# Kernel tuning notes

Hardware: AMD Instinct MI355X
Metric: run time of the kernel (lower is better)

## Reference

```python
import jax, jax.numpy as jnp
import numpy as np

EPS = 1e-5
LOGIT_DIM = 16   # 2**arity, arity=4
HID = 128        # circuit_hidden_dim == pe_dim
MSG = LOGIT_DIM + HID  # 144


def layer_norm(x, scale, bias):
    mu = jnp.mean(x, axis=-1, keepdims=True)
    var = jnp.mean(jnp.square(x - mu), axis=-1, keepdims=True)
    return (x - mu) * jax.lax.rsqrt(var + EPS) * scale + bias


def setup_inputs() -> dict:
    key = jax.random.key(0)
    N = 200000
    ks = jax.random.split(key, 16)
    inp = {
        'logits': jax.random.normal(ks[0], (N, LOGIT_DIM), jnp.float32),
        'hidden': jax.random.normal(ks[1], (N, HID), jnp.float32),
        'layer_pe': jax.random.normal(ks[2], (N, HID), jnp.float32),
        'intra_layer_pe': jax.random.normal(ks[3], (N, HID), jnp.float32),
        'loss': jax.random.normal(ks[4], (N,), jnp.float32),
        'layer': jax.random.randint(ks[5], (N,), 0, 8, jnp.int32),
        'sent_attributes': jax.random.normal(ks[6], (N, MSG), jnp.float32),
    }
    # LayerNorm params (scale=1, bias=0 as flax default init)
    for name, d in [('logits', LOGIT_DIM), ('hidden', HID), ('layer_pe', HID),
                    ('intra_pe', HID), ('loss', 1), ('msg', MSG)]:
        inp[f'ln_{name}_s'] = jnp.ones((d,), jnp.float32)
        inp[f'ln_{name}_b'] = jnp.zeros((d,), jnp.float32)
    # MLP: 545 -> 256 (LN, relu) -> 256 (LN, relu) -> 144
    D_IN = LOGIT_DIM + HID + HID + HID + 1 + MSG  # 545
    inp['W0'] = jax.random.normal(ks[7], (D_IN, 256), jnp.float32) * 0.02
    inp['b0'] = jnp.zeros((256,), jnp.float32)
    inp['mlp_ln0_s'] = jnp.ones((256,), jnp.float32)
    inp['mlp_ln0_b'] = jnp.zeros((256,), jnp.float32)
    inp['W1'] = jax.random.normal(ks[8], (256, 256), jnp.float32) * 0.02
    inp['b1'] = jnp.zeros((256,), jnp.float32)
    inp['mlp_ln1_s'] = jnp.ones((256,), jnp.float32)
    inp['mlp_ln1_b'] = jnp.zeros((256,), jnp.float32)
    inp['W2'] = jax.random.normal(ks[9], (256, MSG), jnp.float32) * 0.02
    inp['b2'] = jnp.zeros((MSG,), jnp.float32)
    return inp


def reference(logits, hidden, layer_pe, intra_layer_pe, loss, layer, sent_attributes,
              ln_logits_s, ln_logits_b, ln_hidden_s, ln_hidden_b,
              ln_layer_pe_s, ln_layer_pe_b, ln_intra_pe_s, ln_intra_pe_b,
              ln_loss_s, ln_loss_b, ln_msg_s, ln_msg_b,
              W0, b0, mlp_ln0_s, mlp_ln0_b, W1, b1, mlp_ln1_s, mlp_ln1_b, W2, b2):
    # Five field-wise LayerNorms + message LayerNorm, then concat
    x = jnp.concatenate([
        layer_norm(logits, ln_logits_s, ln_logits_b),
        layer_norm(hidden, ln_hidden_s, ln_hidden_b),
        layer_norm(layer_pe, ln_layer_pe_s, ln_layer_pe_b),
        layer_norm(intra_layer_pe, ln_intra_pe_s, ln_intra_pe_b),
        layer_norm(loss[:, None], ln_loss_s, ln_loss_b),
        layer_norm(sent_attributes, ln_msg_s, ln_msg_b),
    ], axis=-1)  # [N, 545]
    # MLP: Linear + LN + relu (x2), final Linear
    h = jax.nn.relu(layer_norm(x @ W0 + b0, mlp_ln0_s, mlp_ln0_b))
    h = jax.nn.relu(layer_norm(h @ W1 + b1, mlp_ln1_s, mlp_ln1_b))
    delta = h @ W2 + b2  # [N, 144]
    delta_logits = delta[..., :LOGIT_DIM]
    delta_hidden = delta[..., LOGIT_DIM:]
    # Masked residual: only gate nodes (layer > 0) are updated; scales are 1.0
    mask = (layer > 0)[:, None]
    updated_logits = jnp.where(mask, logits + delta_logits, logits)
    updated_hidden = jnp.where(mask, hidden + delta_hidden, hidden)
    return jnp.concatenate([updated_logits, updated_hidden], axis=-1)  # [N, 144]
```

## Files before the change

kernel.cpp:

```cpp
#include <hip/hip_runtime.h>
#include <hip/hip_bf16.h>

#define EPSV 1e-5f
#define BM   32
#define XSTR 552
#define DSTR 276

using bf16x8 = __attribute__((ext_vector_type(8))) short;
using f32x4  = __attribute__((ext_vector_type(4))) float;
using us4    = __attribute__((ext_vector_type(4))) unsigned short;
using us8    = __attribute__((ext_vector_type(8))) unsigned short;

__device__ __forceinline__ unsigned short f2bf(float f) {
    unsigned int u = __float_as_uint(f);
    u += 0x7fffu + ((u >> 16) & 1u);
    return (unsigned short)(u >> 16);
}

__device__ __forceinline__ int orig_row(int k) {
    return (k < 144) ? k : ((k < 288) ? (k + 257) : (k - 144));
}
__device__ __forceinline__ float seg_pick(int k,
    const float* a, const float* b, const float* c, const float* d, const float* e) {
    if (k < 16)  return a[k];
    if (k < 144) return b[k - 16];
    if (k < 288) return c[k - 144];
    if (k < 416) return d[k - 288];
    return e[k - 416];
}

__global__ void prep_kernel(const float* __restrict__ W0, const float* __restrict__ b0,
                            const float* __restrict__ ln_loss_b,
                            const float* __restrict__ W1, const float* __restrict__ W2,
                            const float* __restrict__ ls_s, const float* __restrict__ hs_s,
                            const float* __restrict__ ms_s, const float* __restrict__ pe_s,
                            const float* __restrict__ in_s,
                            const float* __restrict__ ls_b, const float* __restrict__ hs_b,
                            const float* __restrict__ ms_b, const float* __restrict__ pe_b,
                            const float* __restrict__ in_b,
                            unsigned short* __restrict__ W0p, unsigned short* __restrict__ W1p,
                            unsigned short* __restrict__ W2p, float* __restrict__ b0e)
{
    int gtid = blockIdx.x * blockDim.x + threadIdx.x;
    if (gtid < 17408) {
        int lane = gtid & 63, fid = gtid >> 6;
        int s = fid >> 4, t = fid & 15;
        int n  = (t << 4) + (lane & 15);
        int kb = (s << 5) + ((lane >> 4) << 3);
        us8 v;
        #pragma unroll
        for (int i = 0; i < 8; ++i) {
            int k = kb + i;
            float sc = seg_pick(k, ls_s, hs_s, ms_s, pe_s, in_s);
            v[i] = f2bf(sc * W0[orig_row(k) * 256 + n]);
        }
        *reinterpret_cast<us8*>(W0p + gtid * 8) = v;
    } else if (gtid < 17408 + 8192) {
        int g = gtid - 17408;
        int lane = g & 63, fid = g >> 6;
        int s = fid >> 4, t = fid & 15;
        int n  = (t << 4) + (lane & 15);
        int kb = (s << 5) + ((lane >> 4) << 3);
        us8 v;
        #pragma unroll
        for (int i = 0; i < 8; ++i) v[i] = f2bf(W1[(kb + i) * 256 + n]);
        *reinterpret_cast<us8*>(W1p + g * 8) = v;
    } else if (gtid < 17408 + 8192 + 4608) {
        int g = gtid - 17408 - 8192;
        int lane = g & 63, fid = g >> 6;
        int s = fid / 9, t = fid % 9;
        int n  = (t << 4) + (lane & 15);
        int kb = (s << 5) + ((lane >> 4) << 3);
        us8 v;
        #pragma unroll
        for (int i = 0; i < 8; ++i) v[i] = f2bf(W2[(kb + i) * 144 + n]);
        *reinterpret_cast<us8*>(W2p + g * 8) = v;
    } else if (gtid < 17408 + 8192 + 4608 + 8192) {
        int idx = gtid - (17408 + 8192 + 4608);
        int n   = idx >> 5;
        int sub = idx & 31;
        float acc = 0.f;
        #pragma unroll
        for (int j = 0; j < 17; ++j) {
            int k = sub + 32 * j;
            float bb = seg_pick(k, ls_b, hs_b, ms_b, pe_b, in_b);
            acc += bb * W0[orig_row(k) * 256 + n];
        }
        acc += __shfl_xor(acc, 1);  acc += __shfl_xor(acc, 2);
        acc += __shfl_xor(acc, 4);  acc += __shfl_xor(acc, 8);
        acc += __shfl_xor(acc, 16);
        if (sub == 0)
            b0e[n] = acc + b0[n] + ln_loss_b[0] * W0[400 * 256 + n];
    }
}

template<int L>
__device__ __forceinline__ void stage8(
    const float* __restrict__ src,
    unsigned short* xb, int dstcol, int tid, int row0)
{
    constexpr int SPAN = L / 8;
    const int sub = tid & 7;
    const int r   = tid >> 3;
    const float* p = src + (size_t)(row0 + r) * L + sub * SPAN;
    float ps = 0.f, pq = 0.f;
    if constexpr (SPAN % 4 == 0) {
        constexpr int NV = SPAN / 4;
        float4 v[NV];
        #pragma unroll
        for (int j = 0; j < NV; ++j) {
            v[j] = *reinterpret_cast<const float4*>(p + 4 * j);
            ps += v[j].x + v[j].y + v[j].z + v[j].w;
            pq += v[j].x * v[j].x + v[j].y * v[j].y + v[j].z * v[j].z + v[j].w * v[j].w;
        }
        ps += __shfl_xor(ps, 1); ps += __shfl_xor(ps, 2); ps += __shfl_xor(ps, 4);
        pq += __shfl_xor(pq, 1); pq += __shfl_xor(pq, 2); pq += __shfl_xor(pq, 4);
        const float mu   = ps * (1.f / L);
        const float rstd = rsqrtf(pq * (1.f / L) - mu * mu + EPSV);
        unsigned short* dst = xb + r * XSTR + dstcol + sub * SPAN;
        #pragma unroll
        for (int j = 0; j < NV; ++j) {
            us4 o;
            o[0] = f2bf((v[j].x - mu) * rstd);
            o[1] = f2bf((v[j].y - mu) * rstd);
            o[2] = f2bf((v[j].z - mu) * rstd);
            o[3] = f2bf((v[j].w - mu) * rstd);
            *reinterpret_cast<us4*>(dst + 4 * j) = o;
        }
    } else {
        constexpr int NV = SPAN / 2;
        float2 v[NV];
        #pragma unroll
        for (int j = 0; j < NV; ++j) {
            v[j] = *reinterpret_cast<const float2*>(p + 2 * j);
            ps += v[j].x + v[j].y;
            pq += v[j].x * v[j].x + v[j].y * v[j].y;
        }
        ps += __shfl_xor(ps, 1); ps += __shfl_xor(ps, 2); ps += __shfl_xor(ps, 4);
        pq += __shfl_xor(pq, 1); pq += __shfl_xor(pq, 2); pq += __shfl_xor(pq, 4);
        const float mu   = ps * (1.f / L);
        const float rstd = rsqrtf(pq * (1.f / L) - mu * mu + EPSV);
        unsigned short* dst = xb + r * XSTR + dstcol + sub * SPAN;
        #pragma unroll
        for (int j = 0; j < NV; ++j) {
            unsigned int pk = (unsigned int)f2bf((v[j].x - mu) * rstd)
                            | ((unsigned int)f2bf((v[j].y - mu) * rstd) << 16);
            *reinterpret_cast<unsigned int*>(dst + 2 * j) = pk;
        }
    }
}

__global__ __launch_bounds__(256, 4) void node_update_kernel(
    const float* __restrict__ logits, const float* __restrict__ hidden,
    const float* __restrict__ layer_pe, const float* __restrict__ intra,
    const int* __restrict__ layer, const float* __restrict__ msg,
    const unsigned short* __restrict__ W0p, const float* __restrict__ b0e,
    const float* __restrict__ mlp_ln0_s, const float* __restrict__ mlp_ln0_b,
    const unsigned short* __restrict__ W1p, const float* __restrict__ b1,
    const float* __restrict__ mlp_ln1_s, const float* __restrict__ mlp_ln1_b,
    const unsigned short* __restrict__ W2p, const float* __restrict__ b2,
    float* __restrict__ out)
{
    __shared__ __align__(16) unsigned short sbuf[BM * XSTR];
    __shared__ __align__(16) float redf[BM * 4 * 2];
    __shared__ int lyr[BM];

    float2* redp = reinterpret_cast<float2*>(redf);
    const float4* redq = reinterpret_cast<const float4*>(redf);
    const int tid  = threadIdx.x;
    const int lane = tid & 63;
    const int w    = tid >> 6;
    const int l15  = lane & 15;
    const int lg   = lane >> 4;
    const int row0 = blockIdx.x * BM;

    stage8<16 >(logits,   sbuf,   0, tid, row0);
    stage8<128>(hidden,   sbuf,  16, tid, row0);
    stage8<144>(msg,      sbuf, 144, tid, row0);
    stage8<128>(layer_pe, sbuf, 288, tid, row0);
    stage8<128>(intra,    sbuf, 416, tid, row0);
    if (tid < BM) lyr[tid] = layer[row0 + tid];
    __syncthreads();

    f32x4 acc[2][4];
    #pragma unroll
    for (int m = 0; m < 2; ++m)
        #pragma unroll
        for (int t = 0; t < 4; ++t)
            acc[m][t] = (f32x4){0.f, 0.f, 0.f, 0.f};

    for (int s = 0; s < 17; ++s) {
        bf16x8 a[2];
        #pragma unroll
        for (int m = 0; m < 2; ++m)
            a[m] = *reinterpret_cast<const bf16x8*>(&sbuf[(16 * m + l15) * XSTR + 32 * s + 8 * lg]);
        #pragma unroll
        for (int t = 0; t < 4; ++t) {
            bf16x8 b = *reinterpret_cast<const bf16x8*>(W0p + (((s * 16 + w * 4 + t) * 64 + lane) << 3));
            #pragma unroll
            for (int m = 0; m < 2; ++m)
                acc[m][t] = __builtin_amdgcn_mfma_f32_16x16x32_bf16(a[m], b, acc[m][t], 0, 0, 0);
        }
    }

    {
        float bv[4], sv[4], bb[4];
        #pragma unroll
        for (int t = 0; t < 4; ++t) {
            int n = w * 64 + t * 16 + l15;
            bv[t] = b0e[n]; sv[t] = mlp_ln0_s[n]; bb[t] = mlp_ln0_b[n];
        }
        #pragma unroll
        for (int m = 0; m < 2; ++m)
            #pragma unroll
            for (int t = 0; t < 4; ++t)
                #pragma unroll
                for (int i = 0; i < 4; ++i)
                    acc[m][t][i] += bv[t];
        #pragma unroll
        for (int m = 0; m < 2; ++m) {
            #pragma unroll
            for (int i = 0; i < 4; ++i) {
                float ps = acc[m][0][i] + acc[m][1][i] + acc[m][2][i] + acc[m][3][i];
                float pq = acc[m][0][i] * acc[m][0][i] + acc[m][1][i] * acc[m][1][i]
                         + acc[m][2][i] * acc[m][2][i] + acc[m][3][i] * acc[m][3][i];
                ps += __shfl_xor(ps, 1); ps += __shfl_xor(ps, 2); ps += __shfl_xor(ps, 4); ps += __shfl_xor(ps, 8);
                pq += __shfl_xor(pq, 1); pq += __shfl_xor(pq, 2); pq += __shfl_xor(pq, 4); pq += __shfl_xor(pq, 8);
                if (l15 == 0) redp[(16 * m + 4 * lg + i) * 4 + w] = make_float2(ps, pq);
            }
        }
        __syncthreads();
        #pragma unroll
        for (int m = 0; m < 2; ++m)
            #pragma unroll
            for (int i = 0; i < 4; ++i) {
                int r = 16 * m + 4 * lg + i;
                float4 q0 = redq[r * 2 + 0], q1 = redq[r * 2 + 1];
                float s  = q0.x + q0.z + q1.x + q1.z;
                float q  = q0.y + q0.w + q1.y + q1.w;
                float mu = s * (1.f / 256.f);
                float rstd = rsqrtf(q * (1.f / 256.f) - mu * mu + EPSV);
                #pragma unroll
                for (int t = 0; t < 4; ++t) {
                    float y = (acc[m][t][i] - mu) * rstd * sv[t] + bb[t];
                    sbuf[r * XSTR + w * 64 + t * 16 + l15] = f2bf(fmaxf(y, 0.f));
                }
            }
    }
    __syncthreads();

    #pragma unroll
    for (int m = 0; m < 2; ++m)
        #pragma unroll
        for (int t = 0; t < 4; ++t)
            acc[m][t] = (f32x4){0.f, 0.f, 0.f, 0.f};
    for (int s = 0; s < 8; ++s) {
        bf16x8 a[2];
        #pragma unroll
        for (int m = 0; m < 2; ++m)
            a[m] = *reinterpret_cast<const bf16x8*>(&sbuf[(16 * m + l15) * XSTR + 32 * s + 8 * lg]);
        #pragma unroll
        for (int t = 0; t < 4; ++t) {
            bf16x8 b = *reinterpret_cast<const bf16x8*>(W1p + (((s * 16 + w * 4 + t) * 64 + lane) << 3));
            #pragma unroll
            for (int m = 0; m < 2; ++m)
                acc[m][t] = __builtin_amdgcn_mfma_f32_16x16x32_bf16(a[m], b, acc[m][t], 0, 0, 0);
        }
    }

    {
        float bv[4], sv[4], bb[4];
        #pragma unroll
        for (int t = 0; t < 4; ++t) {
            int n = w * 64 + t * 16 + l15;
            bv[t] = b1[n]; sv[t] = mlp_ln1_s[n]; bb[t] = mlp_ln1_b[n];
        }
        #pragma unroll
        for (int m = 0; m < 2; ++m)
            #pragma unroll
            for (int t = 0; t < 4; ++t)
                #pragma unroll
                for (int i = 0; i < 4; ++i)
                    acc[m][t][i] += bv[t];
        #pragma unroll
        for (int m = 0; m < 2; ++m) {
            #pragma unroll
            for (int i = 0; i < 4; ++i) {
                float ps = acc[m][0][i] + acc[m][1][i] + acc[m][2][i] + acc[m][3][i];
                float pq = acc[m][0][i] * acc[m][0][i] + acc[m][1][i] * acc[m][1][i]
                         + acc[m][2][i] * acc[m][2][i] + acc[m][3][i] * acc[m][3][i];
                ps += __shfl_xor(ps, 1); ps += __shfl_xor(ps, 2); ps += __shfl_xor(ps, 4); ps += __shfl_xor(ps, 8);
                pq += __shfl_xor(pq, 1); pq += __shfl_xor(pq, 2); pq += __shfl_xor(pq, 4); pq += __shfl_xor(pq, 8);
                if (l15 == 0) redp[(16 * m + 4 * lg + i) * 4 + w] = make_float2(ps, pq);
            }
        }
        __syncthreads();
        #pragma unroll
        for (int m = 0; m < 2; ++m)
            #pragma unroll
            for (int i = 0; i < 4; ++i) {
                int r = 16 * m + 4 * lg + i;
                float4 q0 = redq[r * 2 + 0], q1 = redq[r * 2 + 1];
                float s  = q0.x + q0.z + q1.x + q1.z;
                float q  = q0.y + q0.w + q1.y + q1.w;
                float mu = s * (1.f / 256.f);
                float rstd = rsqrtf(q * (1.f / 256.f) - mu * mu + EPSV);
                #pragma unroll
                for (int t = 0; t < 4; ++t) {
                    float y = (acc[m][t][i] - mu) * rstd * sv[t] + bb[t];
                    sbuf[r * XSTR + w * 64 + t * 16 + l15] = f2bf(fmaxf(y, 0.f));
                }
            }
    }
    __syncthreads();

    {
        const int rg = w & 1;
        const int ch = w >> 1;
        const unsigned short* arow = sbuf + (16 * rg + l15) * XSTR;
        float* delta = reinterpret_cast<float*>(sbuf);
        if (ch == 0) {
            f32x4 acc3[5];
            #pragma unroll
            for (int t = 0; t < 5; ++t) acc3[t] = (f32x4){0.f, 0.f, 0.f, 0.f};
            for (int s = 0; s < 8; ++s) {
                bf16x8 a = *reinterpret_cast<const bf16x8*>(arow + 32 * s + 8 * lg);
                #pragma unroll
                for (int t = 0; t < 5; ++t) {
                    bf16x8 b = *reinterpret_cast<const bf16x8*>(W2p + (((s * 9 + t) * 64 + lane) << 3));
                    acc3[t] = __builtin_amdgcn_mfma_f32_16x16x32_bf16(a, b, acc3[t], 0, 0, 0);
                }
            }
            __syncthreads();
            #pragma unroll
            for (int t = 0; t < 5; ++t)
                #pragma unroll
                for (int i = 0; i < 4; ++i)
                    delta[(16 * rg + 4 * lg + i) * DSTR + 16 * t + l15] = acc3[t][i];
        } else {
            f32x4 acc3[4];
            #pragma unroll
            for (int t = 0; t < 4; ++t) acc3[t] = (f32x4){0.f, 0.f, 0.f, 0.f};
            for (int s = 0; s < 8; ++s) {
                bf16x8 a = *reinterpret_cast<const bf16x8*>(arow + 32 * s + 8 * lg);
                #pragma unroll
                for (int t = 0; t < 4; ++t) {
                    bf16x8 b = *reinterpret_cast<const bf16x8*>(W2p + (((s * 9 + t + 5) * 64 + lane) << 3));
                    acc3[t] = __builtin_amdgcn_mfma_f32_16x16x32_bf16(a, b, acc3[t], 0, 0, 0);
                }
            }
            __syncthreads();
            #pragma unroll
            for (int t = 0; t < 4; ++t)
                #pragma unroll
                for (int i = 0; i < 4; ++i)
                    delta[(16 * rg + 4 * lg + i) * DSTR + 16 * (t + 5) + l15] = acc3[t][i];
        }
    }
    __syncthreads();

    const float* delta = reinterpret_cast<const float*>(sbuf);
    #pragma unroll
    for (int j = 0; j < 5; ++j) {
        int idx = tid + j * 256;
        if (idx < BM * 36) {
            int r = idx / 36, c4 = idx % 36;
            int grow = row0 + r;
            float4 d  = *reinterpret_cast<const float4*>(delta + r * DSTR + 4 * c4);
            float4 bb = *reinterpret_cast<const float4*>(b2 + 4 * c4);
            float4 base;
            if (c4 < 4) base = *reinterpret_cast<const float4*>(logits + (size_t)grow * 16 + 4 * c4);
            else        base = *reinterpret_cast<const float4*>(hidden + (size_t)grow * 128 + 4 * c4 - 16);
            const bool mk = lyr[r] > 0;
            f32x4 o;
            o[0] = mk ? base.x + d.x + bb.x : base.x;
            o[1] = mk ? base.y + d.y + bb.y : base.y;
            o[2] = mk ? base.z + d.z + bb.z : base.z;
            o[3] = mk ? base.w + d.w + bb.w : base.w;
            __builtin_nontemporal_store(o, reinterpret_cast<f32x4*>(out + (size_t)grow * 144 + 4 * c4));
        }
    }
}

extern "C" void kernel_launch(void* const* d_in, const int* in_sizes, int n_in,
                              void* d_out, int out_size, void* d_ws, size_t ws_size,
                              hipStream_t stream)
{
    const float* logits        = (const float*)d_in[0];
    const float* hidden        = (const float*)d_in[1];
    const float* layer_pe      = (const float*)d_in[2];
    const float* intra         = (const float*)d_in[3];
    const int*   layer         = (const int*)  d_in[5];
    const float* msg           = (const float*)d_in[6];
    const float* ln_logits_s   = (const float*)d_in[7];
    const float* ln_logits_b   = (const float*)d_in[8];
    const float* ln_hidden_s   = (const float*)d_in[9];
    const float* ln_hidden_b   = (const float*)d_in[10];
    const float* ln_layer_pe_s = (const float*)d_in[11];
    const float* ln_layer_pe_b = (const float*)d_in[12];
    const float* ln_intra_pe_s = (const float*)d_in[13];
    const float* ln_intra_pe_b = (const float*)d_in[14];
    const float* ln_loss_b     = (const float*)d_in[16];
    const float* ln_msg_s      = (const float*)d_in[17];
    const float* ln_msg_b      = (const float*)d_in[18];
    const float* W0            = (const float*)d_in[19];
    const float* b0            = (const float*)d_in[20];
    const float* mlp_ln0_s     = (const float*)d_in[21];
    const float* mlp_ln0_b     = (const float*)d_in[22];
    const float* W1            = (const float*)d_in[23];
    const float* b1            = (const float*)d_in[24];
    const float* mlp_ln1_s     = (const float*)d_in[25];
    const float* mlp_ln1_b     = (const float*)d_in[26];
    const float* W2            = (const float*)d_in[27];
    const float* b2            = (const float*)d_in[28];
    float* out = (float*)d_out;

    unsigned short* W0p = (unsigned short*)d_ws;
    unsigned short* W1p = (unsigned short*)((char*)d_ws + 278528);
    unsigned short* W2p = (unsigned short*)((char*)d_ws + 409600);
    float*          b0e = (float*)((char*)d_ws + 483328);

    prep_kernel<<<150, 256, 0, stream>>>(W0, b0, ln_loss_b, W1, W2,
        ln_logits_s, ln_hidden_s, ln_msg_s, ln_layer_pe_s, ln_intra_pe_s,
        ln_logits_b, ln_hidden_b, ln_msg_b, ln_layer_pe_b, ln_intra_pe_b,
        W0p, W1p, W2p, b0e);

    const int N = in_sizes[5];
    node_update_kernel<<<N / BM, 256, 0, stream>>>(
        logits, hidden, layer_pe, intra, layer, msg,
        W0p, b0e, mlp_ln0_s, mlp_ln0_b,
        W1p, b1, mlp_ln1_s, mlp_ln1_b,
        W2p, b2, out);
}
```

Before: 280.0 us.

## Double block to 512 threads, split N columns across eight waves

The block grows from 4 to 8 waves for the same 32-row tile. Each wave now owns 32 output columns instead of 64 in the first two GEMMs, and the final 144-column GEMM is split 3/2/2/2 tiles across column groups. Staging now uses 16 threads per row with coalesced float4 strides, and the LayerNorm reduction buffer widens to 8 partials per row. The aim is more waves in flight to hide global-load and MFMA latency, at the cost of more barrier participants and reduction overhead.

Measured after the change: 293.5 us. 4.8% more time.

```diff
diff --git a/kernel.cpp b/kernel.cpp
--- a/kernel.cpp
+++ b/kernel.cpp
@@ -95,62 +95,47 @@
 }
 
 template<int L>
-__device__ __forceinline__ void stage8(
+__device__ __forceinline__ void stage16(
     const float* __restrict__ src,
     unsigned short* xb, int dstcol, int tid, int row0)
 {
-    constexpr int SPAN = L / 8;
-    const int sub = tid & 7;
-    const int r   = tid >> 3;
-    const float* p = src + (size_t)(row0 + r) * L + sub * SPAN;
+    constexpr int NJ  = L / 64;
+    constexpr int REM = L - NJ * 64;
+    const int sub = tid & 15;
+    const int r   = tid >> 4;
+    const float* rowp = src + (size_t)(row0 + r) * L;
+    float4 v[NJ > 0 ? NJ : 1];
+    float  vr = 0.f;
     float ps = 0.f, pq = 0.f;
-    if constexpr (SPAN % 4 == 0) {
-        constexpr int NV = SPAN / 4;
-        float4 v[NV];
-        #pragma unroll
-        for (int j = 0; j < NV; ++j) {
-            v[j] = *reinterpret_cast<const float4*>(p + 4 * j);
-            ps += v[j].x + v[j].y + v[j].z + v[j].w;
-            pq += v[j].x * v[j].x + v[j].y * v[j].y + v[j].z * v[j].z + v[j].w * v[j].w;
-        }
-        ps += __shfl_xor(ps, 1); ps += __shfl_xor(ps, 2); ps += __shfl_xor(ps, 4);
-        pq += __shfl_xor(pq, 1); pq += __shfl_xor(pq, 2); pq += __shfl_xor(pq, 4);
-        const float mu   = ps * (1.f / L);
-        const float rstd = rsqrtf(pq * (1.f / L) - mu * mu + EPSV);
-        unsigned short* dst = xb + r * XSTR + dstcol + sub * SPAN;
-        #pragma unroll
-        for (int j = 0; j < NV; ++j) {
-            us4 o;
-            o[0] = f2bf((v[j].x - mu) * rstd);
-            o[1] = f2bf((v[j].y - mu) * rstd);
-            o[2] = f2bf((v[j].z - mu) * rstd);
-            o[3] = f2bf((v[j].w - mu) * rstd);
-            *reinterpret_cast<us4*>(dst + 4 * j) = o;
-        }
-    } else {
-        constexpr int NV = SPAN / 2;
-        float2 v[NV];
-        #pragma unroll
-        for (int j = 0; j < NV; ++j) {
-            v[j] = *reinterpret_cast<const float2*>(p + 2 * j);
-            ps += v[j].x + v[j].y;
-            pq += v[j].x * v[j].x + v[j].y * v[j].y;
-        }
-        ps += __shfl_xor(ps, 1); ps += __shfl_xor(ps, 2); ps += __shfl_xor(ps, 4);
-        pq += __shfl_xor(pq, 1); pq += __shfl_xor(pq, 2); pq += __shfl_xor(pq, 4);
-        const float mu   = ps * (1.f / L);
-        const float rstd = rsqrtf(pq * (1.f / L) - mu * mu + EPSV);
-        unsigned short* dst = xb + r * XSTR + dstcol + sub * SPAN;
-        #pragma unroll
-        for (int j = 0; j < NV; ++j) {
-            unsigned int pk = (unsigned int)f2bf((v[j].x - mu) * rstd)
-                            | ((unsigned int)f2bf((v[j].y - mu) * rstd) << 16);
-            *reinterpret_cast<unsigned int*>(dst + 2 * j) = pk;
-        }
-    }
-}
-
-__global__ __launch_bounds__(256, 4) void node_update_kernel(
+    #pragma unroll
+    for (int j = 0; j < NJ; ++j) {
+        v[j] = *reinterpret_cast<const float4*>(rowp + 4 * sub + 64 * j);
+        ps += v[j].x + v[j].y + v[j].z + v[j].w;
+        pq += v[j].x * v[j].x + v[j].y * v[j].y + v[j].z * v[j].z + v[j].w * v[j].w;
+    }
+    if constexpr (REM) {
+        vr = rowp[64 * NJ + sub];
+        ps += vr; pq += vr * vr;
+    }
+    ps += __shfl_xor(ps, 1); ps += __shfl_xor(ps, 2); ps += __shfl_xor(ps, 4); ps += __shfl_xor(ps, 8);
+    pq += __shfl_xor(pq, 1); pq += __shfl_xor(pq, 2); pq += __shfl_xor(pq, 4); pq += __shfl_xor(pq, 8);
+    const float mu   = ps * (1.f / L);
+    const float rstd = rsqrtf(pq * (1.f / L) - mu * mu + EPSV);
+    unsigned short* dstrow = xb + r * XSTR + dstcol;
+    #pragma unroll
+    for (int j = 0; j < NJ; ++j) {
+        us4 o;
+        o[0] = f2bf((v[j].x - mu) * rstd);
+        o[1] = f2bf((v[j].y - mu) * rstd);
+        o[2] = f2bf((v[j].z - mu) * rstd);
+        o[3] = f2bf((v[j].w - mu) * rstd);
+        *reinterpret_cast<us4*>(dstrow + 4 * sub + 64 * j) = o;
+    }
+    if constexpr (REM)
+        dstrow[64 * NJ + sub] = f2bf((vr - mu) * rstd);
+}
+
+__global__ __launch_bounds__(512, 6) void node_update_kernel(
     const float* __restrict__ logits, const float* __restrict__ hidden,
     const float* __restrict__ layer_pe, const float* __restrict__ intra,
     const int* __restrict__ layer, const float* __restrict__ msg,
@@ -162,7 +147,7 @@
     float* __restrict__ out)
 {
     __shared__ __align__(16) unsigned short sbuf[BM * XSTR];
-    __shared__ __align__(16) float redf[BM * 4 * 2];
+    __shared__ __align__(16) float redf[BM * 8 * 2];
     __shared__ int lyr[BM];
 
     float2* redp = reinterpret_cast<float2*>(redf);
@@ -174,19 +159,19 @@
     const int lg   = lane >> 4;
     const int row0 = blockIdx.x * BM;
 
-    stage8<16 >(logits,   sbuf,   0, tid, row0);
-    stage8<128>(hidden,   sbuf,  16, tid, row0);
-    stage8<144>(msg,      sbuf, 144, tid, row0);
-    stage8<128>(layer_pe, sbuf, 288, tid, row0);
-    stage8<128>(intra,    sbuf, 416, tid, row0);
+    stage16<16 >(logits,   sbuf,   0, tid, row0);
+    stage16<128>(hidden,   sbuf,  16, tid, row0);
+    stage16<144>(msg,      sbuf, 144, tid, row0);
+    stage16<128>(layer_pe, sbuf, 288, tid, row0);
+    stage16<128>(intra,    sbuf, 416, tid, row0);
     if (tid < BM) lyr[tid] = layer[row0 + tid];
     __syncthreads();
 
-    f32x4 acc[2][4];
+    f32x4 acc[2][2];
     #pragma unroll
     for (int m = 0; m < 2; ++m)
         #pragma unroll
-        for (int t = 0; t < 4; ++t)
+        for (int t = 0; t < 2; ++t)
             acc[m][t] = (f32x4){0.f, 0.f, 0.f, 0.f};
 
     for (int s = 0; s < 17; ++s) {
@@ -195,8 +180,8 @@
         for (int m = 0; m < 2; ++m)
             a[m] = *reinterpret_cast<const bf16x8*>(&sbuf[(16 * m + l15) * XSTR + 32 * s + 8 * lg]);
         #pragma unroll
-        for (int t = 0; t < 4; ++t) {
-            bf16x8 b = *reinterpret_cast<const bf16x8*>(W0p + (((s * 16 + w * 4 + t) * 64 + lane) << 3));
+        for (int t = 0; t < 2; ++t) {
+            bf16x8 b = *reinterpret_cast<const bf16x8*>(W0p + (((s * 16 + w * 2 + t) * 64 + lane) << 3));
             #pragma unroll
             for (int m = 0; m < 2; ++m)
                 acc[m][t] = __builtin_amdgcn_mfma_f32_16x16x32_bf16(a[m], b, acc[m][t], 0, 0, 0);
@@ -204,16 +189,16 @@
     }
 
     {
-        float bv[4], sv[4], bb[4];
-        #pragma unroll
-        for (int t = 0; t < 4; ++t) {
-            int n = w * 64 + t * 16 + l15;
+        float bv[2], sv[2], bb[2];
+        #pragma unroll
+        for (int t = 0; t < 2; ++t) {
+            int n = w * 32 + t * 16 + l15;
             bv[t] = b0e[n]; sv[t] = mlp_ln0_s[n]; bb[t] = mlp_ln0_b[n];
         }
         #pragma unroll
         for (int m = 0; m < 2; ++m)
             #pragma unroll
-            for (int t = 0; t < 4; ++t)
+            for (int t = 0; t < 2; ++t)
                 #pragma unroll
                 for (int i = 0; i < 4; ++i)
                     acc[m][t][i] += bv[t];
@@ -221,12 +206,11 @@
         for (int m = 0; m < 2; ++m) {
             #pragma unroll
             for (int i = 0; i < 4; ++i) {
-                float ps = acc[m][0][i] + acc[m][1][i] + acc[m][2][i] + acc[m][3][i];
-                float pq = acc[m][0][i] * acc[m][0][i] + acc[m][1][i] * acc[m][1][i]
-                         + acc[m][2][i] * acc[m][2][i] + acc[m][3][i] * acc[m][3][i];
+                float ps = acc[m][0][i] + acc[m][1][i];
+                float pq = acc[m][0][i] * acc[m][0][i] + acc[m][1][i] * acc[m][1][i];
                 ps += __shfl_xor(ps, 1); ps += __shfl_xor(ps, 2); ps += __shfl_xor(ps, 4); ps += __shfl_xor(ps, 8);
                 pq += __shfl_xor(pq, 1); pq += __shfl_xor(pq, 2); pq += __shfl_xor(pq, 4); pq += __shfl_xor(pq, 8);
-                if (l15 == 0) redp[(16 * m + 4 * lg + i) * 4 + w] = make_float2(ps, pq);
+                if (l15 == 0) redp[(16 * m + 4 * lg + i) * 8 + w] = make_float2(ps, pq);
             }
         }
         __syncthreads();
@@ -235,15 +219,16 @@
             #pragma unroll
             for (int i = 0; i < 4; ++i) {
                 int r = 16 * m + 4 * lg + i;
-                float4 q0 = redq[r * 2 + 0], q1 = redq[r * 2 + 1];
-                float s  = q0.x + q0.z + q1.x + q1.z;
-                float q  = q0.y + q0.w + q1.y + q1.w;
+                float4 q0 = redq[r * 4 + 0], q1 = redq[r * 4 + 1];
+                float4 q2 = redq[r * 4 + 2], q3 = redq[r * 4 + 3];
+                float s  = q0.x + q0.z + q1.x + q1.z + q2.x + q2.z + q3.x + q3.z;
+                float q  = q0.y + q0.w + q1.y + q1.w + q2.y + q2.w + q3.y + q3.w;
                 float mu = s * (1.f / 256.f);
                 float rstd = rsqrtf(q * (1.f / 256.f) - mu * mu + EPSV);
                 #pragma unroll
-                for (int t = 0; t < 4; ++t) {
+                for (int t = 0; t < 2; ++t) {
                     float y = (acc[m][t][i] - mu) * rstd * sv[t] + bb[t];
-                    sbuf[r * XSTR + w * 64 + t * 16 + l15] = f2bf(fmaxf(y, 0.f));
+                    sbuf[r * XSTR + w * 32 + t * 16 + l15] = f2bf(fmaxf(y, 0.f));
                 }
             }
     }
@@ -252,7 +237,7 @@
     #pragma unroll
     for (int m = 0; m < 2; ++m)
         #pragma unroll
-        for (int t = 0; t < 4; ++t)
+        for (int t = 0; t < 2; ++t)
             acc[m][t] = (f32x4){0.f, 0.f, 0.f, 0.f};
     for (int s = 0; s < 8; ++s) {
         bf16x8 a[2];
@@ -260,8 +245,8 @@
         for (int m = 0; m < 2; ++m)
             a[m] = *reinterpret_cast<const bf16x8*>(&sbuf[(16 * m + l15) * XSTR + 32 * s + 8 * lg]);
         #pragma unroll
-        for (int t = 0; t < 4; ++t) {
-            bf16x8 b = *reinterpret_cast<const bf16x8*>(W1p + (((s * 16 + w * 4 + t) * 64 + lane) << 3));
+        for (int t = 0; t < 2; ++t) {
+            bf16x8 b = *reinterpret_cast<const bf16x8*>(W1p + (((s * 16 + w * 2 + t) * 64 + lane) << 3));
             #pragma unroll
             for (int m = 0; m < 2; ++m)
                 acc[m][t] = __builtin_amdgcn_mfma_f32_16x16x32_bf16(a[m], b, acc[m][t], 0, 0, 0);
@@ -269,16 +254,16 @@
     }
 
     {
-        float bv[4], sv[4], bb[4];
-        #pragma unroll
-        for (int t = 0; t < 4; ++t) {
-            int n = w * 64 + t * 16 + l15;
+        float bv[2], sv[2], bb[2];
+        #pragma unroll
+        for (int t = 0; t < 2; ++t) {
+            int n = w * 32 + t * 16 + l15;
             bv[t] = b1[n]; sv[t] = mlp_ln1_s[n]; bb[t] = mlp_ln1_b[n];
         }
         #pragma unroll
         for (int m = 0; m < 2; ++m)
             #pragma unroll
-            for (int t = 0; t < 4; ++t)
+            for (int t = 0; t < 2; ++t)
                 #pragma unroll
                 for (int i = 0; i < 4; ++i)
                     acc[m][t][i] += bv[t];
@@ -286,12 +271,11 @@
         for (int m = 0; m < 2; ++m) {
             #pragma unroll
             for (int i = 0; i < 4; ++i) {
-                float ps = acc[m][0][i] + acc[m][1][i] + acc[m][2][i] + acc[m][3][i];
-                float pq = acc[m][0][i] * acc[m][0][i] + acc[m][1][i] * acc[m][1][i]
-                         + acc[m][2][i] * acc[m][2][i] + acc[m][3][i] * acc[m][3][i];
+                float ps = acc[m][0][i] + acc[m][1][i];
+                float pq = acc[m][0][i] * acc[m][0][i] + acc[m][1][i] * acc[m][1][i];
                 ps += __shfl_xor(ps, 1); ps += __shfl_xor(ps, 2); ps += __shfl_xor(ps, 4); ps += __shfl_xor(ps, 8);
                 pq += __shfl_xor(pq, 1); pq += __shfl_xor(pq, 2); pq += __shfl_xor(pq, 4); pq += __shfl_xor(pq, 8);
-                if (l15 == 0) redp[(16 * m + 4 * lg + i) * 4 + w] = make_float2(ps, pq);
+                if (l15 == 0) redp[(16 * m + 4 * lg + i) * 8 + w] = make_float2(ps, pq);
             }
         }
         __syncthreads();
@@ -300,15 +284,16 @@
             #pragma unroll
             for (int i = 0; i < 4; ++i) {
                 int r = 16 * m + 4 * lg + i;
-                float4 q0 = redq[r * 2 + 0], q1 = redq[r * 2 + 1];
-                float s  = q0.x + q0.z + q1.x + q1.z;
-                float q  = q0.y + q0.w + q1.y + q1.w;
+                float4 q0 = redq[r * 4 + 0], q1 = redq[r * 4 + 1];
+                float4 q2 = redq[r * 4 + 2], q3 = redq[r * 4 + 3];
+                float s  = q0.x + q0.z + q1.x + q1.z + q2.x + q2.z + q3.x + q3.z;
+                float q  = q0.y + q0.w + q1.y + q1.w + q2.y + q2.w + q3.y + q3.w;
                 float mu = s * (1.f / 256.f);
                 float rstd = rsqrtf(q * (1.f / 256.f) - mu * mu + EPSV);
                 #pragma unroll
-                for (int t = 0; t < 4; ++t) {
+                for (int t = 0; t < 2; ++t) {
                     float y = (acc[m][t][i] - mu) * rstd * sv[t] + bb[t];
-                    sbuf[r * XSTR + w * 64 + t * 16 + l15] = f2bf(fmaxf(y, 0.f));
+                    sbuf[r * XSTR + w * 32 + t * 16 + l15] = f2bf(fmaxf(y, 0.f));
                 }
             }
     }
@@ -316,53 +301,54 @@
 
     {
         const int rg = w & 1;
-        const int ch = w >> 1;
+        const int cq = w >> 1;
         const unsigned short* arow = sbuf + (16 * rg + l15) * XSTR;
-        float* delta = reinterpret_cast<float*>(sbuf);
-        if (ch == 0) {
-            f32x4 acc3[5];
-            #pragma unroll
-            for (int t = 0; t < 5; ++t) acc3[t] = (f32x4){0.f, 0.f, 0.f, 0.f};
+        f32x4 acc3[3];
+        #pragma unroll
+        for (int t = 0; t < 3; ++t) acc3[t] = (f32x4){0.f, 0.f, 0.f, 0.f};
+        if (cq == 0) {
             for (int s = 0; s < 8; ++s) {
                 bf16x8 a = *reinterpret_cast<const bf16x8*>(arow + 32 * s + 8 * lg);
                 #pragma unroll
-                for (int t = 0; t < 5; ++t) {
+                for (int t = 0; t < 3; ++t) {
                     bf16x8 b = *reinterpret_cast<const bf16x8*>(W2p + (((s * 9 + t) * 64 + lane) << 3));
                     acc3[t] = __builtin_amdgcn_mfma_f32_16x16x32_bf16(a, b, acc3[t], 0, 0, 0);
                 }
             }
-            __syncthreads();
-            #pragma unroll
-            for (int t = 0; t < 5; ++t)
+        } else {
+            const int tofs = 2 * cq + 1;
+            for (int s = 0; s < 8; ++s) {
+                bf16x8 a = *reinterpret_cast<const bf16x8*>(arow + 32 * s + 8 * lg);
+                #pragma unroll
+                for (int t = 0; t < 2; ++t) {
+                    bf16x8 b = *reinterpret_cast<const bf16x8*>(W2p + (((s * 9 + t + tofs) * 64 + lane) << 3));
+                    acc3[t] = __builtin_amdgcn_mfma_f32_16x16x32_bf16(a, b, acc3[t], 0, 0, 0);
+                }
+            }
+        }
+        __syncthreads();
+        float* delta = reinterpret_cast<float*>(sbuf);
+        if (cq == 0) {
+            #pragma unroll
+            for (int t = 0; t < 3; ++t)
                 #pragma unroll
                 for (int i = 0; i < 4; ++i)
                     delta[(16 * rg + 4 * lg + i) * DSTR + 16 * t + l15] = acc3[t][i];
         } else {
-            f32x4 acc3[4];
-            #pragma unroll
-            for (int t = 0; t < 4; ++t) acc3[t] = (f32x4){0.f, 0.f, 0.f, 0.f};
-            for (int s = 0; s < 8; ++s) {
-                bf16x8 a = *reinterpret_cast<const bf16x8*>(arow + 32 * s + 8 * lg);
-                #pragma unroll
-                for (int t = 0; t < 4; ++t) {
-                    bf16x8 b = *reinterpret_cast<const bf16x8*>(W2p + (((s * 9 + t + 5) * 64 + lane) << 3));
-                    acc3[t] = __builtin_amdgcn_mfma_f32_16x16x32_bf16(a, b, acc3[t], 0, 0, 0);
-                }
-            }
-            __syncthreads();
-            #pragma unroll
-            for (int t = 0; t < 4; ++t)
+            const int tofs = 2 * cq + 1;
+            #pragma unroll
+            for (int t = 0; t < 2; ++t)
                 #pragma unroll
                 for (int i = 0; i < 4; ++i)
-                    delta[(16 * rg + 4 * lg + i) * DSTR + 16 * (t + 5) + l15] = acc3[t][i];
+                    delta[(16 * rg + 4 * lg + i) * DSTR + 16 * (t + tofs) + l15] = acc3[t][i];
         }
     }
     __syncthreads();
 
     const float* delta = reinterpret_cast<const float*>(sbuf);
     #pragma unroll
-    for (int j = 0; j < 5; ++j) {
-        int idx = tid + j * 256;
+    for (int j = 0; j < 3; ++j) {
+        int idx = tid + j * 512;
         if (idx < BM * 36) {
             int r = idx / 36, c4 = idx % 36;
             int grow = row0 + r;
@@ -426,7 +412,7 @@
         W0p, W1p, W2p, b0e);
 
     const int N = in_sizes[5];
-    node_update_kernel<<<N / BM, 256, 0, stream>>>(
+    node_update_kernel<<<N / BM, 512, 0, stream>>>(
         logits, hidden, layer_pe, intra, layer, msg,
         W0p, b0e, mlp_ln0_s, mlp_ln0_b,
         W1p, b1, mlp_ln1_s, mlp_ln1_b,
```
